# Optimization experiments

Hardware: AMD Instinct MI355X
Metric: run time of the kernel (lower is better)

## Reference

```python
import jax, jax.numpy as jnp
import numpy as np

N_NODES = 50000
N_EDGES = 1600000
N_GRAPHS = 64
F_IN = 256
H = 1024
EPS = 1e-5


def setup_inputs() -> dict:
    key = jax.random.key(0)
    ks = jax.random.split(key, 6)
    x = jax.random.normal(ks[0], (N_NODES, F_IN), dtype=jnp.float32)
    edge_index = jax.random.randint(ks[1], (2, N_EDGES), 0, N_NODES, dtype=jnp.int32)
    batch = jnp.sort(jax.random.randint(ks[2], (N_NODES,), 0, N_GRAPHS, dtype=jnp.int32))
    # Glorot-ish init for GCN weights
    W0 = jax.random.normal(ks[3], (F_IN, H), dtype=jnp.float32) * (1.0 / np.sqrt(F_IN))
    b0 = jnp.zeros((H,), dtype=jnp.float32)
    Ws = jax.random.normal(ks[4], (3, H, H), dtype=jnp.float32) * (1.0 / np.sqrt(H))
    bs = jnp.zeros((3, H), dtype=jnp.float32)
    gammas = jnp.ones((4, H), dtype=jnp.float32)
    betas = jnp.zeros((4, H), dtype=jnp.float32)
    return {"x": x, "edge_index": edge_index, "batch": batch,
            "W0": W0, "b0": b0, "Ws": Ws, "bs": bs,
            "gammas": gammas, "betas": betas}


def _gcn_norm(edge_index, n_nodes):
    # Add self-loops (PyG GCNConv default), compute symmetric normalization.
    loops = jnp.arange(n_nodes, dtype=edge_index.dtype)
    row = jnp.concatenate([edge_index[0], loops])  # sources
    col = jnp.concatenate([edge_index[1], loops])  # targets (aggregation index)
    ones = jnp.ones(row.shape[0], dtype=jnp.float32)
    deg = jax.ops.segment_sum(ones, col, num_segments=n_nodes)
    dinv = jnp.where(deg > 0, jax.lax.rsqrt(deg), 0.0)
    norm = dinv[row] * dinv[col]  # [E + N]
    return row, col, norm


def _layer(h, W, b, gamma, beta, row, col, norm):
    ht = h @ W                                           # [N, H] GEMM
    msg = ht[row] * norm[:, None]                        # gather + scale
    agg = jax.ops.segment_sum(msg, col, num_segments=N_NODES) + b
    mu = jnp.mean(agg, axis=-1, keepdims=True)
    var = jnp.mean(jnp.square(agg - mu), axis=-1, keepdims=True)
    hn = (agg - mu) * jax.lax.rsqrt(var + EPS) * gamma + beta
    return jax.nn.relu(hn)


def reference(x, edge_index, batch, W0, b0, Ws, bs, gammas, betas):
    row, col, norm = _gcn_norm(edge_index, N_NODES)
    h = _layer(x, W0, b0, gammas[0], betas[0], row, col, norm)
    for i in range(3):
        h = _layer(h, Ws[i], bs[i], gammas[i + 1], betas[i + 1], row, col, norm)
    # scatter_mean over batch (graph-level pooling)
    sums = jax.ops.segment_sum(h, batch, num_segments=N_GRAPHS)
    cnt = jax.ops.segment_sum(jnp.ones((N_NODES,), jnp.float32), batch, num_segments=N_GRAPHS)
    return sums / jnp.maximum(cnt, 1.0)[:, None]
```

## Files before the change

kernel.cpp:

```cpp
#include <hip/hip_runtime.h>
#include <hip/hip_bf16.h>
#include <stdint.h>

#define NN 50000
#define NE 1600000
#define NG 64
#define FIN 256
#define HD 1024
#define EPSV 1e-5f

typedef __bf16 bf16;
typedef float f32x4 __attribute__((ext_vector_type(4)));
typedef float f32x2 __attribute__((ext_vector_type(2)));
typedef int i32x4 __attribute__((ext_vector_type(4)));

typedef const __attribute__((address_space(1))) void* gptr_as1;
typedef __attribute__((address_space(3))) void* lptr_as3;

__device__ __forceinline__ void load_g2l_16(const void* g, const void* l) {
  __builtin_amdgcn_global_load_lds((gptr_as1)(uintptr_t)g,
                                   (lptr_as3)(uint32_t)(uintptr_t)l, 16, 0, 0);
}

__global__ void hist_kernel(const int* __restrict__ col, int* __restrict__ cnt, int E) {
  int e = blockIdx.x * 256 + threadIdx.x;
  if (e < E) atomicAdd(&cnt[col[e]], 1);
}

__global__ void dinv_kernel(const int* __restrict__ cnt, float* __restrict__ dinv, int n) {
  int i = blockIdx.x * 256 + threadIdx.x;
  if (i < n) dinv[i] = rsqrtf((float)(cnt[i] + 1));
}

__global__ void scan_partial_kernel(const int* __restrict__ cnt, int* __restrict__ partial, int n) {
  __shared__ int red[4];
  int i = blockIdx.x * 256 + threadIdx.x;
  int v = (i < n) ? cnt[i] : 0;
  #pragma unroll
  for (int off = 32; off; off >>= 1) v += __shfl_down(v, off, 64);
  if ((threadIdx.x & 63) == 0) red[threadIdx.x >> 6] = v;
  __syncthreads();
  if (threadIdx.x == 0) partial[blockIdx.x] = red[0] + red[1] + red[2] + red[3];
}

__global__ void scan_scan_kernel(int* __restrict__ partial, int nb) {
  __shared__ int s[256];
  int t = threadIdx.x;
  int v = (t < nb) ? partial[t] : 0;
  s[t] = v;
  __syncthreads();
  for (int off = 1; off < 256; off <<= 1) {
    int x = (t >= off) ? s[t - off] : 0;
    __syncthreads();
    s[t] += x;
    __syncthreads();
  }
  if (t < nb) partial[t] = s[t] - v;
}

__global__ void scan_final_kernel(const int* __restrict__ cnt, const int* __restrict__ partial,
                                  int* __restrict__ row_ptr, int n, int E) {
  __shared__ int s[256];
  int t = threadIdx.x;
  int i = blockIdx.x * 256 + t;
  int v = (i < n) ? cnt[i] : 0;
  s[t] = v;
  __syncthreads();
  for (int off = 1; off < 256; off <<= 1) {
    int x = (t >= off) ? s[t - off] : 0;
    __syncthreads();
    s[t] += x;
    __syncthreads();
  }
  if (i < n) row_ptr[i] = partial[blockIdx.x] + s[t] - v;
  if (i == 0) row_ptr[n] = E;
}

__global__ void scatter_kernel(const int* __restrict__ rowi, const int* __restrict__ coli,
                               const int* __restrict__ row_ptr, int* __restrict__ fill,
                               const float* __restrict__ dinv,
                               int2* __restrict__ csr_sw, int E) {
  int e = blockIdx.x * 256 + threadIdx.x;
  if (e >= E) return;
  int s = rowi[e], d = coli[e];
  int pos = row_ptr[d] + atomicAdd(&fill[d], 1);
  int2 p;
  p.x = s;
  p.y = __float_as_int(dinv[s] * dinv[d]);
  csr_sw[pos] = p;
}

__global__ __launch_bounds__(256) void quant_x_kernel(const float* __restrict__ x,
                                                      uint8_t* __restrict__ X8,
                                                      float* __restrict__ xscale) {
  int row = blockIdx.x * 4 + (threadIdx.x >> 6);
  int t = threadIdx.x & 63;
  float4 v = ((const float4*)(x + (size_t)row * FIN))[t];
  float m = fmaxf(fmaxf(fabsf(v.x), fabsf(v.y)), fmaxf(fabsf(v.z), fabsf(v.w)));
  #pragma unroll
  for (int off = 32; off; off >>= 1) m = fmaxf(m, __shfl_xor(m, off, 64));
  float inv = (m > 0.f) ? 127.0f / m : 0.f;
  int q0 = min(127, max(-127, __float2int_rn(v.x * inv))) + 128;
  int q1 = min(127, max(-127, __float2int_rn(v.y * inv))) + 128;
  int q2 = min(127, max(-127, __float2int_rn(v.z * inv))) + 128;
  int q3 = min(127, max(-127, __float2int_rn(v.w * inv))) + 128;
  uint32_t p = ((uint32_t)q0) | ((uint32_t)q1 << 8) |
               ((uint32_t)q2 << 16) | ((uint32_t)q3 << 24);
  ((uint32_t*)X8)[(size_t)row * 64 + t] = p;
  if (t == 0) xscale[row] = (m > 0.f) ? m / 127.0f : 0.f;
}

__global__ __launch_bounds__(256) void agg0_kernel(
    const uint8_t* __restrict__ X8, const float* __restrict__ xscale,
    const int* __restrict__ row_ptr, const int2* __restrict__ csr_sw,
    const float* __restrict__ dinv,
    int8_t* __restrict__ AX8, float* __restrict__ axscale) {
  const int node = blockIdx.x * 4 + (threadIdx.x >> 6);
  const int t = threadIdx.x & 63;

  float acc[4] = {};
  float sw = 0.f;

  float dn = dinv[node];
  float wself = dn * dn * xscale[node];
  {
    uint32_t d = ((const uint32_t*)X8)[(size_t)node * 64 + t];
    sw += wself;
    acc[0] += wself * (float)(d & 0xffu);
    acc[1] += wself * (float)((d >> 8) & 0xffu);
    acc[2] += wself * (float)((d >> 16) & 0xffu);
    acc[3] += wself * (float)(d >> 24);
  }

  int e = row_ptr[node];
  const int e1 = row_ptr[node + 1];
  for (; e + 4 <= e1; e += 4) {
    int2 p0 = csr_sw[e], p1 = csr_sw[e + 1], p2 = csr_sw[e + 2], p3 = csr_sw[e + 3];
    float w0 = __int_as_float(p0.y) * xscale[p0.x];
    float w1 = __int_as_float(p1.y) * xscale[p1.x];
    float w2 = __int_as_float(p2.y) * xscale[p2.x];
    float w3 = __int_as_float(p3.y) * xscale[p3.x];
    uint32_t d0 = ((const uint32_t*)X8)[(size_t)p0.x * 64 + t];
    uint32_t d1 = ((const uint32_t*)X8)[(size_t)p1.x * 64 + t];
    uint32_t d2 = ((const uint32_t*)X8)[(size_t)p2.x * 64 + t];
    uint32_t d3 = ((const uint32_t*)X8)[(size_t)p3.x * 64 + t];
    sw += w0 + w1 + w2 + w3;
    acc[0] += w0 * (float)(d0 & 0xffu) + w1 * (float)(d1 & 0xffu)
            + w2 * (float)(d2 & 0xffu) + w3 * (float)(d3 & 0xffu);
    acc[1] += w0 * (float)((d0 >> 8) & 0xffu) + w1 * (float)((d1 >> 8) & 0xffu)
            + w2 * (float)((d2 >> 8) & 0xffu) + w3 * (float)((d3 >> 8) & 0xffu);
    acc[2] += w0 * (float)((d0 >> 16) & 0xffu) + w1 * (float)((d1 >> 16) & 0xffu)
            + w2 * (float)((d2 >> 16) & 0xffu) + w3 * (float)((d3 >> 16) & 0xffu);
    acc[3] += w0 * (float)(d0 >> 24) + w1 * (float)(d1 >> 24)
            + w2 * (float)(d2 >> 24) + w3 * (float)(d3 >> 24);
  }
  for (; e < e1; e++) {
    int2 p = csr_sw[e];
    float w = __int_as_float(p.y) * xscale[p.x];
    uint32_t d = ((const uint32_t*)X8)[(size_t)p.x * 64 + t];
    sw += w;
    acc[0] += w * (float)(d & 0xffu);
    acc[1] += w * (float)((d >> 8) & 0xffu);
    acc[2] += w * (float)((d >> 16) & 0xffu);
    acc[3] += w * (float)(d >> 24);
  }

  float c = 128.0f * sw;
  #pragma unroll
  for (int j = 0; j < 4; j++) acc[j] -= c;

  float rm = fmaxf(fmaxf(fabsf(acc[0]), fabsf(acc[1])), fmaxf(fabsf(acc[2]), fabsf(acc[3])));
  #pragma unroll
  for (int off = 32; off; off >>= 1) rm = fmaxf(rm, __shfl_xor(rm, off, 64));
  float qinv = (rm > 0.f) ? 127.0f / rm : 0.f;
  int q0 = min(127, max(-127, __float2int_rn(acc[0] * qinv)));
  int q1 = min(127, max(-127, __float2int_rn(acc[1] * qinv)));
  int q2 = min(127, max(-127, __float2int_rn(acc[2] * qinv)));
  int q3 = min(127, max(-127, __float2int_rn(acc[3] * qinv)));
  uint32_t p = ((uint32_t)(q0 & 0xff)) | ((uint32_t)(q1 & 0xff) << 8) |
               ((uint32_t)(q2 & 0xff) << 16) | ((uint32_t)(q3 & 0xff) << 24);
  ((uint32_t*)AX8)[(size_t)node * 64 + t] = p;
  if (t == 0) axscale[node] = (rm > 0.f) ? rm / 127.0f : 0.f;
}

__global__ __launch_bounds__(256) void ln0_kernel(
    const uint8_t* __restrict__ htu8, const float* __restrict__ scales,
    const float* __restrict__ bias, const float* __restrict__ gamma,
    const float* __restrict__ beta,
    int8_t* __restrict__ hq, float* __restrict__ hscale) {
  const int g = threadIdx.x >> 7;
  const int node = blockIdx.x * 2 + g;
  const int tt = threadIdx.x & 127;
  const int cbL = tt >> 4;
  const int wid = threadIdx.x >> 6;
  __shared__ float red[4];

  float sc = scales[(size_t)node * 8 + cbL];
  uint2 dd = ((const uint2*)(htu8 + (size_t)node * HD))[tt];
  float acc[8];
  acc[0] = sc * ((float)(dd.x & 0xffu) - 128.f);
  acc[1] = sc * ((float)((dd.x >> 8) & 0xffu) - 128.f);
  acc[2] = sc * ((float)((dd.x >> 16) & 0xffu) - 128.f);
  acc[3] = sc * ((float)(dd.x >> 24) - 128.f);
  acc[4] = sc * ((float)(dd.y & 0xffu) - 128.f);
  acc[5] = sc * ((float)((dd.y >> 8) & 0xffu) - 128.f);
  acc[6] = sc * ((float)((dd.y >> 16) & 0xffu) - 128.f);
  acc[7] = sc * ((float)(dd.y >> 24) - 128.f);

  const float4* bias2 = (const float4*)bias;
  float4 ba = bias2[tt * 2], bb = bias2[tt * 2 + 1];
  acc[0] += ba.x; acc[1] += ba.y; acc[2] += ba.z; acc[3] += ba.w;
  acc[4] += bb.x; acc[5] += bb.y; acc[6] += bb.z; acc[7] += bb.w;

  float s = 0.f;
  #pragma unroll
  for (int j = 0; j < 8; j++) s += acc[j];
  #pragma unroll
  for (int off = 32; off; off >>= 1) s += __shfl_down(s, off, 64);
  if ((threadIdx.x & 63) == 0) red[wid] = s;
  __syncthreads();
  float mean = (red[g * 2] + red[g * 2 + 1]) * (1.0f / HD);
  __syncthreads();

  float d[8], s2 = 0.f;
  #pragma unroll
  for (int j = 0; j < 8; j++) { d[j] = acc[j] - mean; s2 += d[j] * d[j]; }
  #pragma unroll
  for (int off = 32; off; off >>= 1) s2 += __shfl_down(s2, off, 64);
  if ((threadIdx.x & 63) == 0) red[wid] = s2;
  __syncthreads();
  float var = (red[g * 2] + red[g * 2 + 1]) * (1.0f / HD);
  float rstd = rsqrtf(var + EPSV);

  const float4* gam2 = (const float4*)gamma;
  const float4* bet2 = (const float4*)beta;
  float4 g0 = gam2[tt * 2], g1 = gam2[tt * 2 + 1];
  float4 be0 = bet2[tt * 2], be1 = bet2[tt * 2 + 1];
  float gv[8] = {g0.x, g0.y, g0.z, g0.w, g1.x, g1.y, g1.z, g1.w};
  float bv[8] = {be0.x, be0.y, be0.z, be0.w, be1.x, be1.y, be1.z, be1.w};
  float o[8];
  float rmax = 0.f;
  #pragma unroll
  for (int j = 0; j < 8; j++) {
    o[j] = fmaxf(d[j] * rstd * gv[j] + bv[j], 0.0f);
    rmax = fmaxf(rmax, o[j]);
  }

  __syncthreads();
  #pragma unroll
  for (int off = 32; off; off >>= 1) rmax = fmaxf(rmax, __shfl_xor(rmax, off, 64));
  if ((threadIdx.x & 63) == 0) red[wid] = rmax;
  __syncthreads();
  float rm = fmaxf(red[g * 2], red[g * 2 + 1]);
  float qinv = (rm > 0.f) ? 127.0f / rm : 0.f;
  int q[8];
  #pragma unroll
  for (int j = 0; j < 8; j++) q[j] = min(127, __float2int_rn(o[j] * qinv));
  uint32_t p0 = ((uint32_t)q[0]) | ((uint32_t)q[1] << 8) | ((uint32_t)q[2] << 16) | ((uint32_t)q[3] << 24);
  uint32_t p1 = ((uint32_t)q[4]) | ((uint32_t)q[5] << 8) | ((uint32_t)q[6] << 16) | ((uint32_t)q[7] << 24);
  uint2 pk; pk.x = p0; pk.y = p1;
  ((uint2*)(hq + (size_t)node * HD))[tt] = pk;
  if (tt == 0) hscale[node] = (rm > 0.f) ? rm / 127.0f : 0.f;
}

__device__ __forceinline__ const float* layer_W(const float* W0, const float* Ws, int L) {
  return (L == 0) ? W0 : Ws + (size_t)(L - 1) * HD * HD;
}

__global__ void wamax_all_kernel(const float* __restrict__ W0, const float* __restrict__ Ws,
                                 uint32_t* __restrict__ colmax) {
  __shared__ float lds[8][32];
  int L = blockIdx.z;
  int K = (L == 0) ? FIN : HD;
  int k0 = blockIdx.y * 128;
  if (k0 >= K) return;
  const float* W = layer_W(W0, Ws, L);
  int n = blockIdx.x * 32 + threadIdx.x;
  int kend = min(k0 + 128, K);
  float m = 0.f;
  for (int k = k0 + threadIdx.y; k < kend; k += 8)
    m = fmaxf(m, fabsf(W[(size_t)k * HD + n]));
  lds[threadIdx.y][threadIdx.x] = m;
  __syncthreads();
  if (threadIdx.y == 0) {
    #pragma unroll
    for (int i = 1; i < 8; i++) m = fmaxf(m, lds[i][threadIdx.x]);
    atomicMax(&colmax[L * HD + n], __float_as_uint(m));
  }
}

__global__ void wscale_all_kernel(const uint32_t* __restrict__ colmax,
                                  float* __restrict__ wscale) {
  int i = blockIdx.x * 256 + threadIdx.x;
  if (i < 4 * HD) {
    float m = __uint_as_float(colmax[i]);
    wscale[i] = (m > 0.f) ? m / 127.0f : 0.f;
  }
}

__global__ void transpose_wq8_all_kernel(const float* __restrict__ W0,
                                         const float* __restrict__ Ws,
                                         const uint32_t* __restrict__ colmax,
                                         int8_t* __restrict__ Wt8_all) {
  __shared__ float tile[32][33];
  int L = blockIdx.z;
  int K = (L == 0) ? FIN : HD;
  int k0 = blockIdx.y * 32;
  if (k0 >= K) return;
  const float* W = layer_W(W0, Ws, L);
  int8_t* Wt8 = Wt8_all + ((L == 0) ? 0 : (size_t)FIN * HD + (size_t)(L - 1) * HD * HD);
  int n0 = blockIdx.x * 32;
  int tx = threadIdx.x, ty = threadIdx.y;
  #pragma unroll
  for (int i = ty; i < 32; i += 8) tile[i][tx] = W[(size_t)(k0 + i) * HD + n0 + tx];
  __syncthreads();
  #pragma unroll
  for (int i = ty; i < 32; i += 8) {
    float cm = __uint_as_float(colmax[L * HD + n0 + i]);
    float inv = (cm > 0.f) ? 127.0f / cm : 0.f;
    int q = min(127, max(-127, __float2int_rn(tile[tx][i] * inv)));
    Wt8[(size_t)(n0 + i) * K + k0 + tx] = (int8_t)q;
  }
}

__global__ __launch_bounds__(256, 4) void gemm_i8_q8_kernel(
    const int8_t* __restrict__ A8, const float* __restrict__ hscale,
    const int8_t* __restrict__ Wt8, const float* __restrict__ wscale,
    uint8_t* __restrict__ C8, float* __restrict__ scales, int M, int K) {
  __shared__ __align__(16) int8_t As[2][128 * 64];
  __shared__ __align__(16) int8_t Bs[2][128 * 64];
  __shared__ float smax[2][128];
  const int tid = threadIdx.x;
  const int w = tid >> 6, l = tid & 63;

  const int nwg = gridDim.x;
  const int o = blockIdx.x;
  const int lid = (o & 7) * (nwg >> 3) + (o >> 3);
  const int m0 = (lid >> 3) * 128, n0 = (lid & 7) * 128;
  const int cb = lid & 7;
  const int wr = w >> 1, wc = w & 1;

  i32x4 acc[4][4] = {};

  const int r0 = tid >> 2;
  const int c16 = (tid & 3) * 16;
  int ar0 = m0 + r0;       if (ar0 >= M) ar0 = M - 1;
  int ar1 = m0 + r0 + 64;  if (ar1 >= M) ar1 = M - 1;
  const int8_t* a0 = A8 + (size_t)ar0 * K + c16;
  const int8_t* a1 = A8 + (size_t)ar1 * K + c16;
  const int8_t* b0 = Wt8 + (size_t)(n0 + r0) * K + c16;
  const int8_t* b1 = Wt8 + (size_t)(n0 + r0 + 64) * K + c16;

  const int mrow = l & 15;
  const int kch = (l >> 4) * 16;

  auto stage = [&](int b, int k) {
    int8_t* asw = &As[b][w * 1024];
    int8_t* bsw = &Bs[b][w * 1024];
    load_g2l_16(a0 + k, asw);
    load_g2l_16(a1 + k, asw + 4096);
    load_g2l_16(b0 + k, bsw);
    load_g2l_16(b1 + k, bsw + 4096);
  };

  const int nit = K >> 6;
  stage(0, 0);
  __syncthreads();

  int cur = 0;
  for (int t = 0; t < nit; ++t) {
    if (t + 1 < nit) stage(cur ^ 1, (t + 1) << 6);
    i32x4 af[4], bf_[4];
    #pragma unroll
    for (int m = 0; m < 4; m++)
      af[m] = *(const i32x4*)&As[cur][(wr * 64 + m * 16 + mrow) * 64 + kch];
    #pragma unroll
    for (int n = 0; n < 4; n++)
      bf_[n] = *(const i32x4*)&Bs[cur][(wc * 64 + n * 16 + mrow) * 64 + kch];
    #pragma unroll
    for (int m = 0; m < 4; m++)
      #pragma unroll
      for (int n = 0; n < 4; n++)
        acc[m][n] = __builtin_amdgcn_mfma_i32_16x16x64_i8(af[m], bf_[n], acc[m][n], 0, 0, 0);
    __syncthreads();
    cur ^= 1;
  }

  float wsv[4];
  #pragma unroll
  for (int n = 0; n < 4; n++) wsv[n] = wscale[n0 + wc * 64 + n * 16 + (l & 15)];

  #pragma unroll
  for (int m = 0; m < 4; m++) {
    #pragma unroll
    for (int r = 0; r < 4; r++) {
      int rl = wr * 64 + m * 16 + (l >> 4) * 4 + r;
      int grow = m0 + rl; if (grow >= M) grow = M - 1;
      float v = 0.f;
      #pragma unroll
      for (int n = 0; n < 4; n++)
        v = fmaxf(v, fabsf((float)acc[m][n][r] * wsv[n]));
      v *= hscale[grow];
      #pragma unroll
      for (int mask = 1; mask < 16; mask <<= 1) v = fmaxf(v, __shfl_xor(v, mask, 64));
      if ((l & 15) == 0) smax[wc][rl] = v;
    }
  }
  __syncthreads();

  #pragma unroll
  for (int m = 0; m < 4; m++) {
    #pragma unroll
    for (int r = 0; r < 4; r++) {
      int rl = wr * 64 + m * 16 + (l >> 4) * 4 + r;
      int grow = m0 + rl;
      float mx = fmaxf(smax[0][rl], smax[1][rl]);
      float inv = (mx > 0.f) ? 127.0f / mx : 0.f;
      if (grow < M) {
        float hs = hscale[grow];
        if (wc == 0 && (l & 15) == 0)
          scales[(size_t)grow * 8 + cb] = (mx > 0.f) ? mx / 127.0f : 0.f;
        #pragma unroll
        for (int n = 0; n < 4; n++) {
          int gcol = n0 + wc * 64 + n * 16 + (l & 15);
          int u = __float2int_rn((float)acc[m][n][r] * hs * wsv[n] * inv) + 128;
          C8[(size_t)grow * HD + gcol] = (uint8_t)u;
        }
      }
    }
  }
}

__device__ __forceinline__ void acc_u8p(f32x2 a[4], float& sw, float w, uint2 d) {
  sw += w;
  f32x2 w2 = {w, w};
  f32x2 v0 = {(float)(d.x & 0xffu), (float)((d.x >> 8) & 0xffu)};
  f32x2 v1 = {(float)((d.x >> 16) & 0xffu), (float)(d.x >> 24)};
  f32x2 v2 = {(float)(d.y & 0xffu), (float)((d.y >> 8) & 0xffu)};
  f32x2 v3 = {(float)((d.y >> 16) & 0xffu), (float)(d.y >> 24)};
  a[0] += w2 * v0;
  a[1] += w2 * v1;
  a[2] += w2 * v2;
  a[3] += w2 * v3;
}

__global__ __launch_bounds__(256) void agg_ln_u8_kernel(
    const uint8_t* __restrict__ htu8, const float* __restrict__ scales,
    const int* __restrict__ row_ptr, const int2* __restrict__ csr_sw,
    const float* __restrict__ dinv, const float* __restrict__ bias,
    const float* __restrict__ gamma, const float* __restrict__ beta,
    int8_t* __restrict__ hq, float* __restrict__ hscale) {
  const int g = threadIdx.x >> 7;
  const int node = blockIdx.x * 2 + g;
  const int tt = threadIdx.x & 127;
  const int cbL = tt >> 4;
  const int wid = threadIdx.x >> 6;
  __shared__ float red[4];

  f32x2 acc2[4] = {};
  float sw = 0.f;

  float dn = dinv[node];
  float wself = dn * dn * scales[(size_t)node * 8 + cbL];
  acc_u8p(acc2, sw, wself, ((const uint2*)(htu8 + (size_t)node * HD))[tt]);

  int e = row_ptr[node];
  const int e1 = row_ptr[node + 1];
  for (; e + 4 <= e1; e += 4) {
    int2 p0 = csr_sw[e], p1 = csr_sw[e + 1], p2 = csr_sw[e + 2], p3 = csr_sw[e + 3];
    float w0 = __int_as_float(p0.y) * scales[(size_t)p0.x * 8 + cbL];
    float w1 = __int_as_float(p1.y) * scales[(size_t)p1.x * 8 + cbL];
    float w2 = __int_as_float(p2.y) * scales[(size_t)p2.x * 8 + cbL];
    float w3 = __int_as_float(p3.y) * scales[(size_t)p3.x * 8 + cbL];
    uint2 d0 = ((const uint2*)(htu8 + (size_t)p0.x * HD))[tt];
    uint2 d1 = ((const uint2*)(htu8 + (size_t)p1.x * HD))[tt];
    uint2 d2 = ((const uint2*)(htu8 + (size_t)p2.x * HD))[tt];
    uint2 d3 = ((const uint2*)(htu8 + (size_t)p3.x * HD))[tt];
    acc_u8p(acc2, sw, w0, d0);
    acc_u8p(acc2, sw, w1, d1);
    acc_u8p(acc2, sw, w2, d2);
    acc_u8p(acc2, sw, w3, d3);
  }
  for (; e < e1; e++) {
    int2 p = csr_sw[e];
    float wgt = __int_as_float(p.y) * scales[(size_t)p.x * 8 + cbL];
    acc_u8p(acc2, sw, wgt, ((const uint2*)(htu8 + (size_t)p.x * HD))[tt]);
  }

  float acc[8] = {acc2[0][0], acc2[0][1], acc2[1][0], acc2[1][1],
                  acc2[2][0], acc2[2][1], acc2[3][0], acc2[3][1]};

  const float4* bias2 = (const float4*)bias;
  float4 ba = bias2[tt * 2], bb = bias2[tt * 2 + 1];
  float c128 = 128.0f * sw;
  acc[0] += ba.x - c128; acc[1] += ba.y - c128; acc[2] += ba.z - c128; acc[3] += ba.w - c128;
  acc[4] += bb.x - c128; acc[5] += bb.y - c128; acc[6] += bb.z - c128; acc[7] += bb.w - c128;

  float s = 0.f;
  #pragma unroll
  for (int j = 0; j < 8; j++) s += acc[j];
  #pragma unroll
  for (int off = 32; off; off >>= 1) s += __shfl_down(s, off, 64);
  if ((threadIdx.x & 63) == 0) red[wid] = s;
  __syncthreads();
  float mean = (red[g * 2] + red[g * 2 + 1]) * (1.0f / HD);
  __syncthreads();

  float d[8], s2 = 0.f;
  #pragma unroll
  for (int j = 0; j < 8; j++) { d[j] = acc[j] - mean; s2 += d[j] * d[j]; }
  #pragma unroll
  for (int off = 32; off; off >>= 1) s2 += __shfl_down(s2, off, 64);
  if ((threadIdx.x & 63) == 0) red[wid] = s2;
  __syncthreads();
  float var = (red[g * 2] + red[g * 2 + 1]) * (1.0f / HD);
  float rstd = rsqrtf(var + EPSV);

  const float4* gam2 = (const float4*)gamma;
  const float4* bet2 = (const float4*)beta;
  float4 g0 = gam2[tt * 2], g1 = gam2[tt * 2 + 1];
  float4 be0 = bet2[tt * 2], be1 = bet2[tt * 2 + 1];
  float gv[8] = {g0.x, g0.y, g0.z, g0.w, g1.x, g1.y, g1.z, g1.w};
  float bv[8] = {be0.x, be0.y, be0.z, be0.w, be1.x, be1.y, be1.z, be1.w};
  float o[8];
  float rmax = 0.f;
  #pragma unroll
  for (int j = 0; j < 8; j++) {
    o[j] = fmaxf(d[j] * rstd * gv[j] + bv[j], 0.0f);
    rmax = fmaxf(rmax, o[j]);
  }

  __syncthreads();
  #pragma unroll
  for (int off = 32; off; off >>= 1) rmax = fmaxf(rmax, __shfl_xor(rmax, off, 64));
  if ((threadIdx.x & 63) == 0) red[wid] = rmax;
  __syncthreads();
  float rm = fmaxf(red[g * 2], red[g * 2 + 1]);
  float qinv = (rm > 0.f) ? 127.0f / rm : 0.f;
  int q[8];
  #pragma unroll
  for (int j = 0; j < 8; j++) q[j] = min(127, __float2int_rn(o[j] * qinv));
  uint32_t p0 = ((uint32_t)q[0]) | ((uint32_t)q[1] << 8) | ((uint32_t)q[2] << 16) | ((uint32_t)q[3] << 24);
  uint32_t p1 = ((uint32_t)q[4]) | ((uint32_t)q[5] << 8) | ((uint32_t)q[6] << 16) | ((uint32_t)q[7] << 24);
  uint2 pk; pk.x = p0; pk.y = p1;
  ((uint2*)(hq + (size_t)node * HD))[tt] = pk;
  if (tt == 0) hscale[node] = (rm > 0.f) ? rm / 127.0f : 0.f;
}

__global__ void starts_kernel(const int* __restrict__ batch, int* __restrict__ start,
                              int n, int ngraph) {
  int g = blockIdx.x * blockDim.x + threadIdx.x;
  if (g > ngraph) return;
  int lo = 0, hi = n;
  while (lo < hi) {
    int mid = (lo + hi) >> 1;
    if (batch[mid] < g) lo = mid + 1; else hi = mid;
  }
  start[g] = lo;
}

#define POOL_CHUNKS 8
__global__ void pool_partial_kernel(const int8_t* __restrict__ hq,
                                    const float* __restrict__ hscale,
                                    const int* __restrict__ start,
                                    float* __restrict__ out) {
  int g = blockIdx.y, c = blockIdx.x;
  int t = threadIdx.x;
  int s0 = start[g], s1 = start[g + 1];
  int len = s1 - s0;
  int per = (len + POOL_CHUNKS - 1) / POOL_CHUNKS;
  int a = s0 + c * per;
  int b = min(a + per, s1);
  if (a >= b) return;
  f32x4 acc = {0.f, 0.f, 0.f, 0.f};
  for (int n = a; n < b; n++) {
    float hs = hscale[n];
    uint32_t d = ((const uint32_t*)(hq + (size_t)n * HD))[t];
    acc[0] += hs * (float)(d & 0xffu);
    acc[1] += hs * (float)((d >> 8) & 0xffu);
    acc[2] += hs * (float)((d >> 16) & 0xffu);
    acc[3] += hs * (float)(d >> 24);
  }
  float* o = out + (size_t)g * HD + t * 4;
  atomicAdd(o + 0, acc[0]);
  atomicAdd(o + 1, acc[1]);
  atomicAdd(o + 2, acc[2]);
  atomicAdd(o + 3, acc[3]);
}

__global__ void pool_div_kernel(float* __restrict__ out, const int* __restrict__ start) {
  int i = blockIdx.x * 256 + threadIdx.x;
  if (i >= NG * HD) return;
  int g = i >> 10;
  float c = (float)max(start[g + 1] - start[g], 1);
  out[i] = out[i] / c;
}

extern "C" void kernel_launch(void* const* d_in, const int* in_sizes, int n_in,
                              void* d_out, int out_size, void* d_ws, size_t ws_size,
                              hipStream_t stream) {
  const float* x      = (const float*)d_in[0];
  const int*   eidx   = (const int*)d_in[1];
  const int*   batch  = (const int*)d_in[2];
  const float* W0     = (const float*)d_in[3];
  const float* b0     = (const float*)d_in[4];
  const float* Ws     = (const float*)d_in[5];
  const float* bs     = (const float*)d_in[6];
  const float* gammas = (const float*)d_in[7];
  const float* betas  = (const float*)d_in[8];
  float* out = (float*)d_out;

  const int* erow = eidx;
  const int* ecol = eidx + NE;

  char* ws = (char*)d_ws;
  size_t off = 0;
  auto alloc = [&](size_t bytes) {
    void* p = ws + off;
    off = (off + bytes + 255) & ~(size_t)255;
    return p;
  };
  int*     cnt     = (int*)alloc((size_t)NN * 4);
  int*     row_ptr = (int*)alloc((size_t)(NN + 1) * 4);
  int*     fill    = (int*)alloc((size_t)NN * 4);
  int*     partial = (int*)alloc(256 * 4);
  float*   dinv    = (float*)alloc((size_t)NN * 4);
  int2*    csr_sw  = (int2*)alloc((size_t)NE * 8);
  int8_t*  Wt8     = (int8_t*)alloc((size_t)FIN * HD + 3 * (size_t)HD * HD);
  int8_t*  A8      = (int8_t*)alloc((size_t)NN * HD);
  uint8_t* ht8     = (uint8_t*)alloc((size_t)NN * HD);
  float*   scales  = (float*)alloc((size_t)NN * 8 * 4);
  uint8_t* X8      = (uint8_t*)alloc((size_t)NN * FIN);
  int8_t*  AX8     = (int8_t*)alloc((size_t)NN * FIN);
  float*   xscale  = (float*)alloc((size_t)NN * 4);
  float*   axscale = (float*)alloc((size_t)NN * 4);
  int*     gstart  = (int*)alloc(65 * 4);

  float*    wscale = (float*)cnt;
  uint32_t* colmax = (uint32_t*)cnt + 4096;
  float*    hscale = (float*)fill;

  hipMemsetAsync(cnt, 0, (size_t)NN * 4, stream);
  hipMemsetAsync(fill, 0, (size_t)NN * 4, stream);
  hipMemsetAsync(out, 0, (size_t)NG * HD * 4, stream);

  hist_kernel<<<(NE + 255) / 256, 256, 0, stream>>>(ecol, cnt, NE);
  dinv_kernel<<<(NN + 255) / 256, 256, 0, stream>>>(cnt, dinv, NN);
  int nb = (NN + 255) / 256;
  scan_partial_kernel<<<nb, 256, 0, stream>>>(cnt, partial, NN);
  scan_scan_kernel<<<1, 256, 0, stream>>>(partial, nb);
  scan_final_kernel<<<nb, 256, 0, stream>>>(cnt, partial, row_ptr, NN, NE);
  scatter_kernel<<<(NE + 255) / 256, 256, 0, stream>>>(erow, ecol, row_ptr, fill, dinv,
                                                       csr_sw, NE);
  starts_kernel<<<1, 128, 0, stream>>>(batch, gstart, NN, NG);

  quant_x_kernel<<<NN / 4, 256, 0, stream>>>(x, X8, xscale);

  hipMemsetAsync(colmax, 0, 4 * HD * 4, stream);
  wamax_all_kernel<<<dim3(HD / 32, 8, 4), dim3(32, 8), 0, stream>>>(W0, Ws, colmax);
  wscale_all_kernel<<<(4 * HD) / 256, 256, 0, stream>>>(colmax, wscale);
  transpose_wq8_all_kernel<<<dim3(HD / 32, HD / 32, 4), dim3(32, 8), 0, stream>>>(
      W0, Ws, colmax, Wt8);

  const int nmt = (NN + 127) / 128;

  agg0_kernel<<<NN / 4, 256, 0, stream>>>(X8, xscale, row_ptr, csr_sw, dinv, AX8, axscale);
  gemm_i8_q8_kernel<<<nmt * 8, 256, 0, stream>>>(AX8, axscale, Wt8, wscale,
                                                 ht8, scales, NN, FIN);
  ln0_kernel<<<NN / 2, 256, 0, stream>>>(ht8, scales, b0, gammas, betas, A8, hscale);

  for (int L = 1; L < 4; L++) {
    const int8_t* WtL = Wt8 + (size_t)FIN * HD + (size_t)(L - 1) * HD * HD;
    const float* bias = bs + (size_t)(L - 1) * HD;
    gemm_i8_q8_kernel<<<nmt * 8, 256, 0, stream>>>(A8, hscale, WtL, wscale + L * HD,
                                                   ht8, scales, NN, HD);
    agg_ln_u8_kernel<<<NN / 2, 256, 0, stream>>>(ht8, scales, row_ptr, csr_sw,
                                                 dinv, bias, gammas + (size_t)L * HD,
                                                 betas + (size_t)L * HD, A8, hscale);
  }

  pool_partial_kernel<<<dim3(POOL_CHUNKS, NG), 256, 0, stream>>>(A8, hscale, gstart, out);
  pool_div_kernel<<<(NG * HD + 255) / 256, 256, 0, stream>>>(out, gstart);
}
```

Baseline: 1.411 ms.

## Map one wavefront per node in aggregation+LN kernel with 16-byte gathers

The aggregation+layernorm kernel now gives each node a single 64-lane wavefront instead of two wavefronts. Each lane gathers 16 bytes per neighbor rather than 8, and the row reductions use xor shuffles only, so the LDS round trips and block barriers are gone. Separately, the dinv computation is folded into the scan kernel, and the column-max pass is replaced by a single kernel without atomics or a memset. The cost is more registers per lane (16 accumulators) and fewer waves in flight per node, which may reduce latency hiding for the irregular neighbor gathers.

```diff
diff --git a/kernel.cpp b/kernel.cpp
--- a/kernel.cpp
+++ b/kernel.cpp
@@ -11,7 +11,6 @@
 
 typedef __bf16 bf16;
 typedef float f32x4 __attribute__((ext_vector_type(4)));
-typedef float f32x2 __attribute__((ext_vector_type(2)));
 typedef int i32x4 __attribute__((ext_vector_type(4)));
 
 typedef const __attribute__((address_space(1))) void* gptr_as1;
@@ -25,11 +24,6 @@
 __global__ void hist_kernel(const int* __restrict__ col, int* __restrict__ cnt, int E) {
   int e = blockIdx.x * 256 + threadIdx.x;
   if (e < E) atomicAdd(&cnt[col[e]], 1);
-}
-
-__global__ void dinv_kernel(const int* __restrict__ cnt, float* __restrict__ dinv, int n) {
-  int i = blockIdx.x * 256 + threadIdx.x;
-  if (i < n) dinv[i] = rsqrtf((float)(cnt[i] + 1));
 }
 
 __global__ void scan_partial_kernel(const int* __restrict__ cnt, int* __restrict__ partial, int n) {
@@ -59,7 +53,8 @@
 }
 
 __global__ void scan_final_kernel(const int* __restrict__ cnt, const int* __restrict__ partial,
-                                  int* __restrict__ row_ptr, int n, int E) {
+                                  int* __restrict__ row_ptr, float* __restrict__ dinv,
+                                  int n, int E) {
   __shared__ int s[256];
   int t = threadIdx.x;
   int i = blockIdx.x * 256 + t;
@@ -72,7 +67,10 @@
     s[t] += x;
     __syncthreads();
   }
-  if (i < n) row_ptr[i] = partial[blockIdx.x] + s[t] - v;
+  if (i < n) {
+    row_ptr[i] = partial[blockIdx.x] + s[t] - v;
+    dinv[i] = rsqrtf((float)(v + 1));
+  }
   if (i == 0) row_ptr[n] = E;
 }
 
@@ -267,40 +265,29 @@
   return (L == 0) ? W0 : Ws + (size_t)(L - 1) * HD * HD;
 }
 
-__global__ void wamax_all_kernel(const float* __restrict__ W0, const float* __restrict__ Ws,
-                                 uint32_t* __restrict__ colmax) {
+__global__ void wamax_full_kernel(const float* __restrict__ W0, const float* __restrict__ Ws,
+                                  float* __restrict__ colmaxf, float* __restrict__ wscale) {
   __shared__ float lds[8][32];
-  int L = blockIdx.z;
+  int L = blockIdx.y;
   int K = (L == 0) ? FIN : HD;
-  int k0 = blockIdx.y * 128;
-  if (k0 >= K) return;
   const float* W = layer_W(W0, Ws, L);
   int n = blockIdx.x * 32 + threadIdx.x;
-  int kend = min(k0 + 128, K);
   float m = 0.f;
-  for (int k = k0 + threadIdx.y; k < kend; k += 8)
+  for (int k = threadIdx.y; k < K; k += 8)
     m = fmaxf(m, fabsf(W[(size_t)k * HD + n]));
   lds[threadIdx.y][threadIdx.x] = m;
   __syncthreads();
   if (threadIdx.y == 0) {
     #pragma unroll
     for (int i = 1; i < 8; i++) m = fmaxf(m, lds[i][threadIdx.x]);
-    atomicMax(&colmax[L * HD + n], __float_as_uint(m));
-  }
-}
-
-__global__ void wscale_all_kernel(const uint32_t* __restrict__ colmax,
-                                  float* __restrict__ wscale) {
-  int i = blockIdx.x * 256 + threadIdx.x;
-  if (i < 4 * HD) {
-    float m = __uint_as_float(colmax[i]);
-    wscale[i] = (m > 0.f) ? m / 127.0f : 0.f;
+    colmaxf[L * HD + n] = m;
+    wscale[L * HD + n] = (m > 0.f) ? m / 127.0f : 0.f;
   }
 }
 
 __global__ void transpose_wq8_all_kernel(const float* __restrict__ W0,
                                          const float* __restrict__ Ws,
-                                         const uint32_t* __restrict__ colmax,
+                                         const float* __restrict__ colmaxf,
                                          int8_t* __restrict__ Wt8_all) {
   __shared__ float tile[32][33];
   int L = blockIdx.z;
@@ -316,7 +303,7 @@
   __syncthreads();
   #pragma unroll
   for (int i = ty; i < 32; i += 8) {
-    float cm = __uint_as_float(colmax[L * HD + n0 + i]);
+    float cm = colmaxf[L * HD + n0 + i];
     float inv = (cm > 0.f) ? 127.0f / cm : 0.f;
     int q = min(127, max(-127, __float2int_rn(tile[tx][i] * inv)));
     Wt8[(size_t)(n0 + i) * K + k0 + tx] = (int8_t)q;
@@ -431,38 +418,34 @@
   }
 }
 
-__device__ __forceinline__ void acc_u8p(f32x2 a[4], float& sw, float w, uint2 d) {
-  sw += w;
-  f32x2 w2 = {w, w};
-  f32x2 v0 = {(float)(d.x & 0xffu), (float)((d.x >> 8) & 0xffu)};
-  f32x2 v1 = {(float)((d.x >> 16) & 0xffu), (float)(d.x >> 24)};
-  f32x2 v2 = {(float)(d.y & 0xffu), (float)((d.y >> 8) & 0xffu)};
-  f32x2 v3 = {(float)((d.y >> 16) & 0xffu), (float)(d.y >> 24)};
-  a[0] += w2 * v0;
-  a[1] += w2 * v1;
-  a[2] += w2 * v2;
-  a[3] += w2 * v3;
-}
-
 __global__ __launch_bounds__(256) void agg_ln_u8_kernel(
     const uint8_t* __restrict__ htu8, const float* __restrict__ scales,
     const int* __restrict__ row_ptr, const int2* __restrict__ csr_sw,
     const float* __restrict__ dinv, const float* __restrict__ bias,
     const float* __restrict__ gamma, const float* __restrict__ beta,
     int8_t* __restrict__ hq, float* __restrict__ hscale) {
-  const int g = threadIdx.x >> 7;
-  const int node = blockIdx.x * 2 + g;
-  const int tt = threadIdx.x & 127;
-  const int cbL = tt >> 4;
-  const int wid = threadIdx.x >> 6;
-  __shared__ float red[4];
-
-  f32x2 acc2[4] = {};
+  const int node = blockIdx.x * 4 + (threadIdx.x >> 6);
+  const int l = threadIdx.x & 63;
+  const int cbL = l >> 3;
+
+  float acc[16] = {};
   float sw = 0.f;
+
+  auto ACC = [&](float w, const uint4& dd) {
+    sw += w;
+    const uint32_t dw[4] = {dd.x, dd.y, dd.z, dd.w};
+    #pragma unroll
+    for (int c = 0; c < 4; c++) {
+      acc[4 * c + 0] += w * (float)(dw[c] & 0xffu);
+      acc[4 * c + 1] += w * (float)((dw[c] >> 8) & 0xffu);
+      acc[4 * c + 2] += w * (float)((dw[c] >> 16) & 0xffu);
+      acc[4 * c + 3] += w * (float)(dw[c] >> 24);
+    }
+  };
 
   float dn = dinv[node];
   float wself = dn * dn * scales[(size_t)node * 8 + cbL];
-  acc_u8p(acc2, sw, wself, ((const uint2*)(htu8 + (size_t)node * HD))[tt]);
+  ACC(wself, ((const uint4*)(htu8 + (size_t)node * HD))[l]);
 
   int e = row_ptr[node];
   const int e1 = row_ptr[node + 1];
@@ -472,79 +455,79 @@
     float w1 = __int_as_float(p1.y) * scales[(size_t)p1.x * 8 + cbL];
     float w2 = __int_as_float(p2.y) * scales[(size_t)p2.x * 8 + cbL];
     float w3 = __int_as_float(p3.y) * scales[(size_t)p3.x * 8 + cbL];
-    uint2 d0 = ((const uint2*)(htu8 + (size_t)p0.x * HD))[tt];
-    uint2 d1 = ((const uint2*)(htu8 + (size_t)p1.x * HD))[tt];
-    uint2 d2 = ((const uint2*)(htu8 + (size_t)p2.x * HD))[tt];
-    uint2 d3 = ((const uint2*)(htu8 + (size_t)p3.x * HD))[tt];
-    acc_u8p(acc2, sw, w0, d0);
-    acc_u8p(acc2, sw, w1, d1);
-    acc_u8p(acc2, sw, w2, d2);
-    acc_u8p(acc2, sw, w3, d3);
+    uint4 d0 = ((const uint4*)(htu8 + (size_t)p0.x * HD))[l];
+    uint4 d1 = ((const uint4*)(htu8 + (size_t)p1.x * HD))[l];
+    uint4 d2 = ((const uint4*)(htu8 + (size_t)p2.x * HD))[l];
+    uint4 d3 = ((const uint4*)(htu8 + (size_t)p3.x * HD))[l];
+    ACC(w0, d0);
+    ACC(w1, d1);
+    ACC(w2, d2);
+    ACC(w3, d3);
   }
   for (; e < e1; e++) {
     int2 p = csr_sw[e];
     float wgt = __int_as_float(p.y) * scales[(size_t)p.x * 8 + cbL];
-    acc_u8p(acc2, sw, wgt, ((const uint2*)(htu8 + (size_t)p.x * HD))[tt]);
-  }
-
-  float acc[8] = {acc2[0][0], acc2[0][1], acc2[1][0], acc2[1][1],
-                  acc2[2][0], acc2[2][1], acc2[3][0], acc2[3][1]};
-
-  const float4* bias2 = (const float4*)bias;
-  float4 ba = bias2[tt * 2], bb = bias2[tt * 2 + 1];
+    ACC(wgt, ((const uint4*)(htu8 + (size_t)p.x * HD))[l]);
+  }
+
+  const float4* bias4 = (const float4*)bias;
   float c128 = 128.0f * sw;
-  acc[0] += ba.x - c128; acc[1] += ba.y - c128; acc[2] += ba.z - c128; acc[3] += ba.w - c128;
-  acc[4] += bb.x - c128; acc[5] += bb.y - c128; acc[6] += bb.z - c128; acc[7] += bb.w - c128;
+  #pragma unroll
+  for (int c = 0; c < 4; c++) {
+    float4 bb = bias4[l * 4 + c];
+    acc[4 * c + 0] += bb.x - c128;
+    acc[4 * c + 1] += bb.y - c128;
+    acc[4 * c + 2] += bb.z - c128;
+    acc[4 * c + 3] += bb.w - c128;
+  }
 
   float s = 0.f;
   #pragma unroll
-  for (int j = 0; j < 8; j++) s += acc[j];
-  #pragma unroll
-  for (int off = 32; off; off >>= 1) s += __shfl_down(s, off, 64);
-  if ((threadIdx.x & 63) == 0) red[wid] = s;
-  __syncthreads();
-  float mean = (red[g * 2] + red[g * 2 + 1]) * (1.0f / HD);
-  __syncthreads();
-
-  float d[8], s2 = 0.f;
-  #pragma unroll
-  for (int j = 0; j < 8; j++) { d[j] = acc[j] - mean; s2 += d[j] * d[j]; }
-  #pragma unroll
-  for (int off = 32; off; off >>= 1) s2 += __shfl_down(s2, off, 64);
-  if ((threadIdx.x & 63) == 0) red[wid] = s2;
-  __syncthreads();
-  float var = (red[g * 2] + red[g * 2 + 1]) * (1.0f / HD);
-  float rstd = rsqrtf(var + EPSV);
-
-  const float4* gam2 = (const float4*)gamma;
-  const float4* bet2 = (const float4*)beta;
-  float4 g0 = gam2[tt * 2], g1 = gam2[tt * 2 + 1];
-  float4 be0 = bet2[tt * 2], be1 = bet2[tt * 2 + 1];
-  float gv[8] = {g0.x, g0.y, g0.z, g0.w, g1.x, g1.y, g1.z, g1.w};
-  float bv[8] = {be0.x, be0.y, be0.z, be0.w, be1.x, be1.y, be1.z, be1.w};
-  float o[8];
+  for (int j = 0; j < 16; j++) s += acc[j];
+  #pragma unroll
+  for (int off = 32; off; off >>= 1) s += __shfl_xor(s, off, 64);
+  float mean = s * (1.0f / HD);
+
+  float d[16], s2 = 0.f;
+  #pragma unroll
+  for (int j = 0; j < 16; j++) { d[j] = acc[j] - mean; s2 += d[j] * d[j]; }
+  #pragma unroll
+  for (int off = 32; off; off >>= 1) s2 += __shfl_xor(s2, off, 64);
+  float rstd = rsqrtf(s2 * (1.0f / HD) + EPSV);
+
+  const float4* gam4 = (const float4*)gamma;
+  const float4* bet4 = (const float4*)beta;
+  float o[16];
   float rmax = 0.f;
   #pragma unroll
-  for (int j = 0; j < 8; j++) {
-    o[j] = fmaxf(d[j] * rstd * gv[j] + bv[j], 0.0f);
-    rmax = fmaxf(rmax, o[j]);
-  }
-
-  __syncthreads();
+  for (int c = 0; c < 4; c++) {
+    float4 gg = gam4[l * 4 + c];
+    float4 be = bet4[l * 4 + c];
+    float gv[4] = {gg.x, gg.y, gg.z, gg.w};
+    float bv[4] = {be.x, be.y, be.z, be.w};
+    #pragma unroll
+    for (int j = 0; j < 4; j++) {
+      float v = fmaxf(d[4 * c + j] * rstd * gv[j] + bv[j], 0.0f);
+      o[4 * c + j] = v;
+      rmax = fmaxf(rmax, v);
+    }
+  }
   #pragma unroll
   for (int off = 32; off; off >>= 1) rmax = fmaxf(rmax, __shfl_xor(rmax, off, 64));
-  if ((threadIdx.x & 63) == 0) red[wid] = rmax;
-  __syncthreads();
-  float rm = fmaxf(red[g * 2], red[g * 2 + 1]);
-  float qinv = (rm > 0.f) ? 127.0f / rm : 0.f;
-  int q[8];
-  #pragma unroll
-  for (int j = 0; j < 8; j++) q[j] = min(127, __float2int_rn(o[j] * qinv));
-  uint32_t p0 = ((uint32_t)q[0]) | ((uint32_t)q[1] << 8) | ((uint32_t)q[2] << 16) | ((uint32_t)q[3] << 24);
-  uint32_t p1 = ((uint32_t)q[4]) | ((uint32_t)q[5] << 8) | ((uint32_t)q[6] << 16) | ((uint32_t)q[7] << 24);
-  uint2 pk; pk.x = p0; pk.y = p1;
-  ((uint2*)(hq + (size_t)node * HD))[tt] = pk;
-  if (tt == 0) hscale[node] = (rm > 0.f) ? rm / 127.0f : 0.f;
+  float qinv = (rmax > 0.f) ? 127.0f / rmax : 0.f;
+
+  uint32_t pw[4];
+  #pragma unroll
+  for (int c = 0; c < 4; c++) {
+    int q0 = min(127, __float2int_rn(o[4 * c + 0] * qinv));
+    int q1 = min(127, __float2int_rn(o[4 * c + 1] * qinv));
+    int q2 = min(127, __float2int_rn(o[4 * c + 2] * qinv));
+    int q3 = min(127, __float2int_rn(o[4 * c + 3] * qinv));
+    pw[c] = ((uint32_t)q0) | ((uint32_t)q1 << 8) | ((uint32_t)q2 << 16) | ((uint32_t)q3 << 24);
+  }
+  uint4 pk; pk.x = pw[0]; pk.y = pw[1]; pk.z = pw[2]; pk.w = pw[3];
+  ((uint4*)(hq + (size_t)node * HD))[l] = pk;
+  if (l == 0) hscale[node] = (rmax > 0.f) ? rmax / 127.0f : 0.f;
 }
 
 __global__ void starts_kernel(const int* __restrict__ batch, int* __restrict__ start,
@@ -636,31 +619,28 @@
   float*   axscale = (float*)alloc((size_t)NN * 4);
   int*     gstart  = (int*)alloc(65 * 4);
 
-  float*    wscale = (float*)cnt;
-  uint32_t* colmax = (uint32_t*)cnt + 4096;
-  float*    hscale = (float*)fill;
+  float* wscale  = (float*)cnt;
+  float* colmaxf = (float*)cnt + 4096;
+  float* hscale  = (float*)fill;
 
   hipMemsetAsync(cnt, 0, (size_t)NN * 4, stream);
   hipMemsetAsync(fill, 0, (size_t)NN * 4, stream);
   hipMemsetAsync(out, 0, (size_t)NG * HD * 4, stream);
 
   hist_kernel<<<(NE + 255) / 256, 256, 0, stream>>>(ecol, cnt, NE);
-  dinv_kernel<<<(NN + 255) / 256, 256, 0, stream>>>(cnt, dinv, NN);
   int nb = (NN + 255) / 256;
   scan_partial_kernel<<<nb, 256, 0, stream>>>(cnt, partial, NN);
   scan_scan_kernel<<<1, 256, 0, stream>>>(partial, nb);
-  scan_final_kernel<<<nb, 256, 0, stream>>>(cnt, partial, row_ptr, NN, NE);
+  scan_final_kernel<<<nb, 256, 0, stream>>>(cnt, partial, row_ptr, dinv, NN, NE);
   scatter_kernel<<<(NE + 255) / 256, 256, 0, stream>>>(erow, ecol, row_ptr, fill, dinv,
                                                        csr_sw, NE);
   starts_kernel<<<1, 128, 0, stream>>>(batch, gstart, NN, NG);
 
   quant_x_kernel<<<NN / 4, 256, 0, stream>>>(x, X8, xscale);
 
-  hipMemsetAsync(colmax, 0, 4 * HD * 4, stream);
-  wamax_all_kernel<<<dim3(HD / 32, 8, 4), dim3(32, 8), 0, stream>>>(W0, Ws, colmax);
-  wscale_all_kernel<<<(4 * HD) / 256, 256, 0, stream>>>(colmax, wscale);
+  wamax_full_kernel<<<dim3(HD / 32, 4), dim3(32, 8), 0, stream>>>(W0, Ws, colmaxf, wscale);
   transpose_wq8_all_kernel<<<dim3(HD / 32, HD / 32, 4), dim3(32, 8), 0, stream>>>(
-      W0, Ws, colmax, Wt8);
+      W0, Ws, colmaxf, Wt8);
 
   const int nmt = (NN + 127) / 128;
 
@@ -674,7 +654,7 @@
     const float* bias = bs + (size_t)(L - 1) * HD;
     gemm_i8_q8_kernel<<<nmt * 8, 256, 0, stream>>>(A8, hscale, WtL, wscale + L * HD,
                                                    ht8, scales, NN, HD);
-    agg_ln_u8_kernel<<<NN / 2, 256, 0, stream>>>(ht8, scales, row_ptr, csr_sw,
+    agg_ln_u8_kernel<<<NN / 4, 256, 0, stream>>>(ht8, scales, row_ptr, csr_sw,
                                                  dinv, bias, gammas + (size_t)L * HD,
                                                  betas + (size_t)L * HD, A8, hscale);
   }
```

Result: no change. 1.412 ms (median of 2 runs) (+0.1%).
